# Performance work log

Measured on AMD Instinct MI355X. Metric: run time of the kernel, lower is better.

## Reference

```python
import jax, jax.numpy as jnp
import numpy as np

N_NODES = 100000
N_EDGES = 1600000
IN_C = 128
HID_C = 64
HEADS = 2
OUT_C = 40
NEG_SLOPE = 0.2  # PyG GATConv default


def setup_inputs() -> dict:
    key = jax.random.key(0)
    ks = jax.random.split(key, 10)
    x = jax.random.normal(ks[0], (N_NODES, IN_C), dtype=jnp.float32)
    edge_index = jax.random.randint(ks[1], (2, N_EDGES), 0, N_NODES, dtype=jnp.int32)
    # layer 1 params: Linear(in, heads*hid), att_src/att_dst [heads, hid], bias [heads*hid]
    s1 = 1.0 / np.sqrt(IN_C)
    W1 = jax.random.uniform(ks[2], (IN_C, HEADS * HID_C), minval=-s1, maxval=s1, dtype=jnp.float32)
    att_src1 = jax.random.normal(ks[3], (HEADS, HID_C), dtype=jnp.float32) * 0.1
    att_dst1 = jax.random.normal(ks[4], (HEADS, HID_C), dtype=jnp.float32) * 0.1
    b1 = jnp.zeros((HEADS * HID_C,), dtype=jnp.float32)
    # layer 2 params: Linear(heads*hid, out), heads=1, concat=False
    s2 = 1.0 / np.sqrt(HEADS * HID_C)
    W2 = jax.random.uniform(ks[5], (HEADS * HID_C, OUT_C), minval=-s2, maxval=s2, dtype=jnp.float32)
    att_src2 = jax.random.normal(ks[6], (1, OUT_C), dtype=jnp.float32) * 0.1
    att_dst2 = jax.random.normal(ks[7], (1, OUT_C), dtype=jnp.float32) * 0.1
    b2 = jnp.zeros((OUT_C,), dtype=jnp.float32)
    return {"x": x, "edge_index": edge_index, "W1": W1, "att_src1": att_src1,
            "att_dst1": att_dst1, "b1": b1, "W2": W2, "att_src2": att_src2,
            "att_dst2": att_dst2, "b2": b2}


def _gat_conv(x, src, dst, n, W, a_src, a_dst):
    # x: [N, F_in]; W: [F_in, H*C]; a_src/a_dst: [H, C]
    H, C = a_src.shape
    h = (x @ W).reshape(n, H, C)                       # [N, H, C]
    alpha_src = jnp.einsum('nhc,hc->nh', h, a_src)     # [N, H]
    alpha_dst = jnp.einsum('nhc,hc->nh', h, a_dst)
    e = alpha_src[src] + alpha_dst[dst]                # [E, H]
    e = jax.nn.leaky_relu(e, NEG_SLOPE)
    # numerically stable softmax over edges grouped by destination node
    m = jax.ops.segment_max(e, dst, num_segments=n)    # [N, H]
    ex = jnp.exp(e - m[dst])
    s = jax.ops.segment_sum(ex, dst, num_segments=n)
    coef = ex / (s[dst] + 1e-16)                       # [E, H]
    msg = h[src] * coef[:, :, None]                    # [E, H, C]
    return jax.ops.segment_sum(msg, dst, num_segments=n)  # [N, H, C]


def reference(x, edge_index, W1, att_src1, att_dst1, b1, W2, att_src2, att_dst2, b2):
    n = x.shape[0]
    # PyG GATConv adds self-loops by default
    loops = jnp.arange(n, dtype=edge_index.dtype)
    src = jnp.concatenate([edge_index[0], loops])
    dst = jnp.concatenate([edge_index[1], loops])
    # layer 1: heads=2, concat -> [N, H*C] + bias, then ELU
    h1 = _gat_conv(x, src, dst, n, W1, att_src1, att_dst1)
    h1 = h1.reshape(n, -1) + b1
    h1 = jax.nn.elu(h1)
    # layer 2: heads=1, concat=False -> mean over heads (=squeeze) + bias
    h2 = _gat_conv(h1, src, dst, n, W2, att_src2, att_dst2)
    h2 = h2.mean(axis=1) + b2
    return jax.nn.log_softmax(h2, axis=1)
```

## Files before the change

kernel.cpp:

```cpp
#include <hip/hip_runtime.h>
#include <hip/hip_fp16.h>
#include <math.h>

#define N_NODES 100000
#define N_EDGES 1600000
#define E_TOT   (N_EDGES + N_NODES)

#define NB     512
#define NPB    196
#define BCAP   4096
#define BIN_CH 4096
#define NBIN_WG ((E_TOT + BIN_CH - 1) / BIN_CH)

typedef __attribute__((ext_vector_type(8))) short short8v;
typedef __attribute__((ext_vector_type(4))) float float4v;

__device__ __forceinline__ float wexp(float v) {
    v = v > 0.f ? v : 0.2f * v;
    return __expf(v);
}

__device__ __forceinline__ unsigned short f2bf(float f) {
    unsigned u = __float_as_uint(f);
    return (unsigned short)((u + 0x7FFFu + ((u >> 16) & 1u)) >> 16);
}

__global__ __launch_bounds__(256) void xprep_k(
    const float* __restrict__ x, unsigned short* __restrict__ xb)
{
    int gid = blockIdx.x * 256 + threadIdx.x;
    float4 v = ((const float4*)x)[gid];
    ushort4 o;
    o.x = f2bf(v.x); o.y = f2bf(v.y); o.z = f2bf(v.z); o.w = f2bf(v.w);
    ((ushort4*)xb)[gid] = o;
}

__global__ __launch_bounds__(256) void w1prep_k(
    const float* __restrict__ W1, unsigned short* __restrict__ W1b)
{
    for (int idx = threadIdx.x; idx < 16384; idx += 256) {
        int i    = idx & 7;
        int lane = (idx >> 3) & 63;
        int f    = (idx >> 9) & 7;
        int ks   = idx >> 12;
        int k   = ks * 32 + (lane >> 4) * 8 + i;
        int col = f * 16 + (lane & 15);
        W1b[idx] = f2bf(W1[k * 128 + col]);
    }
}

__global__ __launch_bounds__(256) void gemm1_k(
    const unsigned short* __restrict__ xb, const unsigned short* __restrict__ W1b,
    const float* __restrict__ as1, const float* __restrict__ ad1,
    __half* __restrict__ h1h, float* __restrict__ asrc, float* __restrict__ adst)
{
    const int t = threadIdx.x;
    const int w = t >> 6, L = t & 63;
    const int lr = L & 15;
    const int lg = L >> 4;
    const int nbase = blockIdx.x * 64 + w * 16;

    float4v acc[8];
#pragma unroll
    for (int f = 0; f < 8; ++f) acc[f] = (float4v)0.f;

    int arow = nbase + lr; if (arow >= N_NODES) arow = N_NODES - 1;
    const unsigned short* xrow = xb + (size_t)arow * 128 + lg * 8;

#pragma unroll
    for (int ks = 0; ks < 4; ++ks) {
        short8v a = *(const short8v*)(xrow + ks * 32);
        const unsigned short* wb = W1b + ((size_t)ks * 8 * 64 + L) * 8;
#pragma unroll
        for (int f = 0; f < 8; ++f) {
            short8v b = *(const short8v*)(wb + (size_t)f * 512);
            acc[f] = __builtin_amdgcn_mfma_f32_16x16x32_bf16(a, b, acc[f], 0, 0, 0);
        }
    }

    float as_v[8], ad_v[8];
#pragma unroll
    for (int f = 0; f < 8; ++f) {
        as_v[f] = as1[f * 16 + lr];
        ad_v[f] = ad1[f * 16 + lr];
    }

#pragma unroll
    for (int r = 0; r < 4; ++r) {
        int node = nbase + lg * 4 + r;
        bool ok = node < N_NODES;
        if (ok) {
#pragma unroll
            for (int f = 0; f < 8; ++f)
                h1h[(size_t)node * 128 + f * 16 + lr] = __float2half_rn(acc[f][r]);
        }
        float ps0 = 0.f, pd0 = 0.f, ps1 = 0.f, pd1 = 0.f;
#pragma unroll
        for (int f = 0; f < 4; ++f) { ps0 += acc[f][r] * as_v[f]; pd0 += acc[f][r] * ad_v[f]; }
#pragma unroll
        for (int f = 4; f < 8; ++f) { ps1 += acc[f][r] * as_v[f]; pd1 += acc[f][r] * ad_v[f]; }
#pragma unroll
        for (int off = 1; off < 16; off <<= 1) {
            ps0 += __shfl_xor(ps0, off); pd0 += __shfl_xor(pd0, off);
            ps1 += __shfl_xor(ps1, off); pd1 += __shfl_xor(pd1, off);
        }
        if (lr == 0 && ok) {
            asrc[node * 2 + 0] = ps0; asrc[node * 2 + 1] = ps1;
            adst[node * 2 + 0] = pd0; adst[node * 2 + 1] = pd1;
        }
    }
}

__global__ __launch_bounds__(256) void bin_k(
    const int* __restrict__ ei, int* __restrict__ bcur, unsigned* __restrict__ bdata)
{
    __shared__ int hist[NB];
    __shared__ int base[NB];
    const int t = threadIdx.x;
    const int e0 = blockIdx.x * BIN_CH;

    int rs[16], rd[16];
#pragma unroll
    for (int p = 0; p < 16; ++p) {
        int e = e0 + p * 256 + t;
        if (e < E_TOT) {
            if (e < N_EDGES) { rs[p] = ei[e]; rd[p] = ei[N_EDGES + e]; }
            else             { rs[p] = rd[p] = e - N_EDGES; }
        } else rd[p] = -1;
    }

    for (int b = t; b < NB; b += 256) hist[b] = 0;
    __syncthreads();

#pragma unroll
    for (int p = 0; p < 16; ++p)
        if (rd[p] >= 0) atomicAdd(&hist[rd[p] / NPB], 1);
    __syncthreads();

    for (int b = t; b < NB; b += 256) {
        int c = hist[b];
        base[b] = c ? atomicAdd(&bcur[b], c) : 0;
        hist[b] = 0;
    }
    __syncthreads();

#pragma unroll
    for (int p = 0; p < 16; ++p) {
        if (rd[p] < 0) continue;
        int b  = rd[p] / NPB;
        int dl = rd[p] - b * NPB;
        int pos = base[b] + atomicAdd(&hist[b], 1);
        if (pos < BCAP)
            bdata[(size_t)b * BCAP + pos] = (unsigned)rs[p] | ((unsigned)dl << 17);
    }
}

__global__ __launch_bounds__(512) void scanb_k(
    const int* __restrict__ bcur, int* __restrict__ bbase)
{
    __shared__ int a[NB], b_[NB];
    int t = threadIdx.x;
    int v = bcur[t];
    a[t] = v;
    __syncthreads();
    int* src = a; int* dst = b_;
    for (int off = 1; off < NB; off <<= 1) {
        dst[t] = (t >= off) ? src[t - off] + src[t] : src[t];
        __syncthreads();
        int* tmp = src; src = dst; dst = tmp;
    }
    bbase[t] = src[t] - v;
}

__global__ __launch_bounds__(256) void build_k(
    const unsigned* __restrict__ bdata, const int* __restrict__ bcur,
    const int* __restrict__ bbase, int* __restrict__ row_start,
    int* __restrict__ csr_src)
{
    __shared__ unsigned rec[BCAP];
    __shared__ int hist[256];
    __shared__ int excl[NPB];
    __shared__ int lcur[NPB];
    const int t = threadIdx.x;
    const int b = blockIdx.x;
    const int cnt = min(bcur[b], BCAP);
    const int bb = bbase[b];

    hist[t] = 0;
    if (t < NPB) lcur[t] = 0;
    __syncthreads();

    for (int i = t; i < cnt; i += 256) {
        unsigned r = bdata[(size_t)b * BCAP + i];
        rec[i] = r;
        atomicAdd(&hist[r >> 17], 1);
    }
    __syncthreads();

    int v = hist[t];
    __syncthreads();
    for (int off = 1; off < 256; off <<= 1) {
        int y = (t >= off) ? hist[t - off] : 0;
        __syncthreads();
        hist[t] += y;
        __syncthreads();
    }
    if (t < NPB) excl[t] = hist[t] - v;
    __syncthreads();

    int node = b * NPB + t;
    if (t < NPB && node <= N_NODES) row_start[node] = bb + excl[t];

    for (int i = t; i < cnt; i += 256) {
        unsigned r = rec[i];
        int dl = r >> 17;
        int s  = r & 0x1FFFF;
        int slot = atomicAdd(&lcur[dl], 1);
        csr_src[bb + excl[dl] + slot] = s;
    }
}

__global__ __launch_bounds__(256) void fagg1_k(
    const int* __restrict__ csr_src, const int* __restrict__ row_start,
    const float* __restrict__ asrc, const float* __restrict__ adst,
    const __half* __restrict__ h1h, const float* __restrict__ b1,
    __half* __restrict__ out1h)
{
    int node = blockIdx.x * 4 + (threadIdx.x >> 6);
    int L = threadIdx.x & 63;
    int h = L >> 5;
    int b = row_start[node], e = row_start[node + 1];
    const float* as_h = asrc + h;
    float ad = adst[node * 2 + h];
    const __half2* H = (const __half2*)h1h;

    float2 a0 = make_float2(0.f, 0.f), a1 = a0, a2 = a0, a3 = a0;
    float d0 = 0.f, d1 = 0.f, d2 = 0.f, d3 = 0.f;

    int j = b;
    for (; j + 3 < e; j += 4) {
        int s0 = csr_src[j], s1 = csr_src[j + 1], s2 = csr_src[j + 2], s3 = csr_src[j + 3];
        float w0 = wexp(as_h[s0 * 2] + ad);
        float w1 = wexp(as_h[s1 * 2] + ad);
        float w2 = wexp(as_h[s2 * 2] + ad);
        float w3 = wexp(as_h[s3 * 2] + ad);
        float2 x0 = __half22float2(H[(size_t)s0 * 64 + L]);
        float2 x1 = __half22float2(H[(size_t)s1 * 64 + L]);
        float2 x2 = __half22float2(H[(size_t)s2 * 64 + L]);
        float2 x3 = __half22float2(H[(size_t)s3 * 64 + L]);
        a0.x += w0 * x0.x; a0.y += w0 * x0.y; d0 += w0;
        a1.x += w1 * x1.x; a1.y += w1 * x1.y; d1 += w1;
        a2.x += w2 * x2.x; a2.y += w2 * x2.y; d2 += w2;
        a3.x += w3 * x3.x; a3.y += w3 * x3.y; d3 += w3;
    }
    for (; j < e; ++j) {
        int s = csr_src[j];
        float w = wexp(as_h[s * 2] + ad);
        float2 xv = __half22float2(H[(size_t)s * 64 + L]);
        a0.x += w * xv.x; a0.y += w * xv.y; d0 += w;
    }

    float inv = 1.f / (((d0 + d1) + (d2 + d3)) + 1e-16f);
    float2 bb = ((const float2*)b1)[L];
    float vx = (a0.x + a1.x + a2.x + a3.x) * inv + bb.x;
    float vy = (a0.y + a1.y + a2.y + a3.y) * inv + bb.y;
    vx = vx > 0.f ? vx : expm1f(vx);
    vy = vy > 0.f ? vy : expm1f(vy);
    ((__half2*)(out1h + (size_t)node * 128))[L] = __floats2half2_rn(vx, vy);
}

__global__ __launch_bounds__(256) void gemm2_k(
    const __half* __restrict__ in1h, const float* __restrict__ W2,
    const float* __restrict__ as2, const float* __restrict__ ad2,
    __half* __restrict__ h2h, float* __restrict__ asrc, float* __restrict__ adst)
{
    __shared__ float xs[64][65];
    __shared__ float Wsh[64][64];
    __shared__ float as_s[64], ad_s[64];
    const int t = threadIdx.x;
    const int nbase = blockIdx.x * 64;
    const int c4 = t & 15;
    const int ng = t >> 4;

    if (t < 64) {
        as_s[t] = (t < 40) ? as2[t] : 0.f;
        ad_s[t] = (t < 40) ? ad2[t] : 0.f;
    }

    float acc[4][4];
#pragma unroll
    for (int i = 0; i < 4; ++i)
#pragma unroll
        for (int j = 0; j < 4; ++j) acc[i][j] = 0.f;

    for (int kt = 0; kt < 128; kt += 64) {
        __syncthreads();
        {
            int r = t >> 4;
            int c = (t & 15) * 4;
#pragma unroll
            for (int p = 0; p < 4; ++p) {
                int row = p * 16 + r;
                int gr = nbase + row; if (gr > N_NODES - 1) gr = N_NODES - 1;
                const __half2* src = (const __half2*)(in1h + (size_t)gr * 128 + kt + c);
                float2 f01 = __half22float2(src[0]);
                float2 f23 = __half22float2(src[1]);
                xs[row][c + 0] = f01.x; xs[row][c + 1] = f01.y;
                xs[row][c + 2] = f23.x; xs[row][c + 3] = f23.y;
            }
        }
        for (int i = t; i < 4096; i += 256) {
            int k = i >> 6, c = i & 63;
            Wsh[k][c] = (c < 40) ? W2[(size_t)(kt + k) * 40 + c] : 0.f;
        }
        __syncthreads();

#pragma unroll 4
        for (int k = 0; k < 64; ++k) {
            float4 w = *(const float4*)&Wsh[k][c4 * 4];
            float x0 = xs[ng * 4 + 0][k], x1 = xs[ng * 4 + 1][k];
            float x2 = xs[ng * 4 + 2][k], x3 = xs[ng * 4 + 3][k];
            acc[0][0] += x0 * w.x; acc[0][1] += x0 * w.y; acc[0][2] += x0 * w.z; acc[0][3] += x0 * w.w;
            acc[1][0] += x1 * w.x; acc[1][1] += x1 * w.y; acc[1][2] += x1 * w.z; acc[1][3] += x1 * w.w;
            acc[2][0] += x2 * w.x; acc[2][1] += x2 * w.y; acc[2][2] += x2 * w.z; acc[2][3] += x2 * w.w;
            acc[3][0] += x3 * w.x; acc[3][1] += x3 * w.y; acc[3][2] += x3 * w.z; acc[3][3] += x3 * w.w;
        }
    }

    float4 as4 = *(const float4*)&as_s[c4 * 4];
    float4 ad4 = *(const float4*)&ad_s[c4 * 4];
#pragma unroll
    for (int i = 0; i < 4; ++i) {
        int node = nbase + ng * 4 + i;
        float axx = acc[i][0], ayy = acc[i][1], azz = acc[i][2], aww = acc[i][3];
        if (node < N_NODES) {
            __half2* row = (__half2*)(h2h + (size_t)node * 64);
            row[2 * c4]     = __floats2half2_rn(axx, ayy);
            row[2 * c4 + 1] = __floats2half2_rn(azz, aww);
        }
        float ps = axx * as4.x + ayy * as4.y + azz * as4.z + aww * as4.w;
        float pd = axx * ad4.x + ayy * ad4.y + azz * ad4.z + aww * ad4.w;
#pragma unroll
        for (int off = 1; off < 16; off <<= 1) {
            ps += __shfl_xor(ps, off);
            pd += __shfl_xor(pd, off);
        }
        if ((t & 15) == 0 && node < N_NODES) {
            asrc[node] = ps;
            adst[node] = pd;
        }
    }
}

__global__ __launch_bounds__(256) void fagg2_k(
    const int* __restrict__ csr_src, const int* __restrict__ row_start,
    const float* __restrict__ asrc, const float* __restrict__ adst,
    const __half* __restrict__ h2h, const float* __restrict__ b2,
    float* __restrict__ out)
{
    int node = blockIdx.x * 4 + (threadIdx.x >> 6);
    int L = threadIdx.x & 63;
    bool act = L < 40;
    int col = act ? L : 0;
    int b = row_start[node], e = row_start[node + 1];
    float ad = adst[node];

    float a0 = 0.f, a1 = 0.f, a2 = 0.f, a3 = 0.f;
    float d0 = 0.f, d1 = 0.f, d2 = 0.f, d3 = 0.f;

    int j = b;
    for (; j + 3 < e; j += 4) {
        int s0 = csr_src[j], s1 = csr_src[j + 1], s2 = csr_src[j + 2], s3 = csr_src[j + 3];
        float w0 = wexp(asrc[s0] + ad);
        float w1 = wexp(asrc[s1] + ad);
        float w2 = wexp(asrc[s2] + ad);
        float w3 = wexp(asrc[s3] + ad);
        float x0 = __half2float(h2h[(size_t)s0 * 64 + col]);
        float x1 = __half2float(h2h[(size_t)s1 * 64 + col]);
        float x2 = __half2float(h2h[(size_t)s2 * 64 + col]);
        float x3 = __half2float(h2h[(size_t)s3 * 64 + col]);
        a0 += w0 * x0; d0 += w0;
        a1 += w1 * x1; d1 += w1;
        a2 += w2 * x2; d2 += w2;
        a3 += w3 * x3; d3 += w3;
    }
    for (; j < e; ++j) {
        int s = csr_src[j];
        float w = wexp(asrc[s] + ad);
        float xv = __half2float(h2h[(size_t)s * 64 + col]);
        a0 += w * xv; d0 += w;
    }

    float den = (d0 + d1) + (d2 + d3);
    float acc = (a0 + a1) + (a2 + a3);
    float v = act ? acc / (den + 1e-16f) + b2[L] : -1e30f;
    float mx = v;
#pragma unroll
    for (int off = 32; off; off >>= 1) mx = fmaxf(mx, __shfl_xor(mx, off));
    float ex = act ? __expf(v - mx) : 0.f;
#pragma unroll
    for (int off = 32; off; off >>= 1) ex += __shfl_xor(ex, off);
    if (act) out[(size_t)node * 40 + L] = v - mx - logf(ex);
}

extern "C" void kernel_launch(void* const* d_in, const int* in_sizes, int n_in,
                              void* d_out, int out_size, void* d_ws, size_t ws_size,
                              hipStream_t stream)
{
    const float* x   = (const float*)d_in[0];
    const int*   ei  = (const int*)d_in[1];
    const float* W1  = (const float*)d_in[2];
    const float* as1 = (const float*)d_in[3];
    const float* ad1 = (const float*)d_in[4];
    const float* b1  = (const float*)d_in[5];
    const float* W2  = (const float*)d_in[6];
    const float* as2 = (const float*)d_in[7];
    const float* ad2 = (const float*)d_in[8];
    const float* b2  = (const float*)d_in[9];
    float* out = (float*)d_out;

    float* ws = (float*)d_ws;
    __half* h1h   = (__half*)ws;
    __half* out1h = (__half*)(ws + 6400000);
    float* asrc1 = ws + 19200000;
    float* adst1 = ws + 19400000;
    float* asrc2 = ws + 19600000;
    float* adst2 = ws + 19700000;
    int* bcur      = (int*)(ws + 20110000);
    int* bbase     = (int*)(ws + 20111000);
    int* row_start = (int*)(ws + 20112000);
    int* csr_src   = (int*)(ws + 20220000);
    unsigned* bdata = (unsigned*)(ws + 22000000);
    unsigned short* xb  = (unsigned short*)(ws + 24100000);
    unsigned short* W1b = (unsigned short*)(ws + 27300000);

    hipMemsetAsync(bcur, 0, NB * sizeof(int), stream);

    xprep_k<<<12500, 256, 0, stream>>>(x, xb);
    w1prep_k<<<1, 256, 0, stream>>>(W1, W1b);

    bin_k<<<NBIN_WG, 256, 0, stream>>>(ei, bcur, bdata);
    scanb_k<<<1, 512, 0, stream>>>(bcur, bbase);
    build_k<<<NB, 256, 0, stream>>>(bdata, bcur, bbase, row_start, csr_src);

    gemm1_k<<<1563, 256, 0, stream>>>(xb, W1b, as1, ad1, h1h, asrc1, adst1);
    fagg1_k<<<25000, 256, 0, stream>>>(csr_src, row_start, asrc1, adst1, h1h, b1, out1h);

    __half* h2h = h1h;
    gemm2_k<<<1563, 256, 0, stream>>>(out1h, W2, as2, ad2, h2h, asrc2, adst2);
    fagg2_k<<<25000, 256, 0, stream>>>(csr_src, row_start, asrc2, adst2, h2h, b2, out);
}
```

Measured before the change: 286.1 us.

## Store node features in column panels and aggregate per panel for cache locality

The GEMM outputs are now written as column panels: 8 panels of 16 halves for layer 1 and 8 panels of 8 halves for layer 2. Each aggregation block processes only one panel, so the gathered working set per pass is small enough to stay in cache. Lanes also split edges across slots and finish with a shuffle reduction. The grid grows 8x, which recomputes edge weights and rereads the CSR arrays once per panel. Layer 2 adds a separate final kernel for bias and log-softmax, with an extra intermediate buffer round trip.

Result: slower. 856.4 us (+199.3%).

```diff
diff --git a/kernel.cpp b/kernel.cpp
--- a/kernel.cpp
+++ b/kernel.cpp
@@ -11,6 +11,9 @@
 #define BCAP   4096
 #define BIN_CH 4096
 #define NBIN_WG ((E_TOT + BIN_CH - 1) / BIN_CH)
+
+#define PAN1 (N_NODES * 16)
+#define PAN2 (N_NODES * 8)
 
 typedef __attribute__((ext_vector_type(8))) short short8v;
 typedef __attribute__((ext_vector_type(4))) float float4v;
@@ -52,7 +55,7 @@
 __global__ __launch_bounds__(256) void gemm1_k(
     const unsigned short* __restrict__ xb, const unsigned short* __restrict__ W1b,
     const float* __restrict__ as1, const float* __restrict__ ad1,
-    __half* __restrict__ h1h, float* __restrict__ asrc, float* __restrict__ adst)
+    __half* __restrict__ h1p, float* __restrict__ asrc, float* __restrict__ adst)
 {
     const int t = threadIdx.x;
     const int w = t >> 6, L = t & 63;
@@ -92,7 +95,7 @@
         if (ok) {
 #pragma unroll
             for (int f = 0; f < 8; ++f)
-                h1h[(size_t)node * 128 + f * 16 + lr] = __float2half_rn(acc[f][r]);
+                h1p[(size_t)f * PAN1 + (size_t)node * 16 + lr] = __float2half_rn(acc[f][r]);
         }
         float ps0 = 0.f, pd0 = 0.f, ps1 = 0.f, pd1 = 0.f;
 #pragma unroll
@@ -186,6 +189,8 @@
     const int cnt = min(bcur[b], BCAP);
     const int bb = bbase[b];
 
+    if (b == 0 && t < 16) csr_src[E_TOT + t] = 0;
+
     hist[t] = 0;
     if (t < NPB) lcur[t] = 0;
     __syncthreads();
@@ -223,56 +228,43 @@
 __global__ __launch_bounds__(256) void fagg1_k(
     const int* __restrict__ csr_src, const int* __restrict__ row_start,
     const float* __restrict__ asrc, const float* __restrict__ adst,
-    const __half* __restrict__ h1h, const float* __restrict__ b1,
+    const __half* __restrict__ h1p, const float* __restrict__ b1,
     __half* __restrict__ out1h)
 {
-    int node = blockIdx.x * 4 + (threadIdx.x >> 6);
-    int L = threadIdx.x & 63;
-    int h = L >> 5;
-    int b = row_start[node], e = row_start[node + 1];
+    const int slice = blockIdx.x & 7;
+    const int node = (blockIdx.x >> 3) * 4 + (threadIdx.x >> 6);
+    const int L = threadIdx.x & 63;
+    const int eslot = L >> 4, c16 = L & 15;
+    const int col = slice * 16 + c16;
+    const int h = col >> 6;
+    const int b = row_start[node], e = row_start[node + 1];
+    const float ad = adst[node * 2 + h];
     const float* as_h = asrc + h;
-    float ad = adst[node * 2 + h];
-    const __half2* H = (const __half2*)h1h;
-
-    float2 a0 = make_float2(0.f, 0.f), a1 = a0, a2 = a0, a3 = a0;
-    float d0 = 0.f, d1 = 0.f, d2 = 0.f, d3 = 0.f;
-
-    int j = b;
-    for (; j + 3 < e; j += 4) {
-        int s0 = csr_src[j], s1 = csr_src[j + 1], s2 = csr_src[j + 2], s3 = csr_src[j + 3];
-        float w0 = wexp(as_h[s0 * 2] + ad);
-        float w1 = wexp(as_h[s1 * 2] + ad);
-        float w2 = wexp(as_h[s2 * 2] + ad);
-        float w3 = wexp(as_h[s3 * 2] + ad);
-        float2 x0 = __half22float2(H[(size_t)s0 * 64 + L]);
-        float2 x1 = __half22float2(H[(size_t)s1 * 64 + L]);
-        float2 x2 = __half22float2(H[(size_t)s2 * 64 + L]);
-        float2 x3 = __half22float2(H[(size_t)s3 * 64 + L]);
-        a0.x += w0 * x0.x; a0.y += w0 * x0.y; d0 += w0;
-        a1.x += w1 * x1.x; a1.y += w1 * x1.y; d1 += w1;
-        a2.x += w2 * x2.x; a2.y += w2 * x2.y; d2 += w2;
-        a3.x += w3 * x3.x; a3.y += w3 * x3.y; d3 += w3;
-    }
-    for (; j < e; ++j) {
-        int s = csr_src[j];
-        float w = wexp(as_h[s * 2] + ad);
-        float2 xv = __half22float2(H[(size_t)s * 64 + L]);
-        a0.x += w * xv.x; a0.y += w * xv.y; d0 += w;
-    }
-
-    float inv = 1.f / (((d0 + d1) + (d2 + d3)) + 1e-16f);
-    float2 bb = ((const float2*)b1)[L];
-    float vx = (a0.x + a1.x + a2.x + a3.x) * inv + bb.x;
-    float vy = (a0.y + a1.y + a2.y + a3.y) * inv + bb.y;
-    vx = vx > 0.f ? vx : expm1f(vx);
-    vy = vy > 0.f ? vy : expm1f(vy);
-    ((__half2*)(out1h + (size_t)node * 128))[L] = __floats2half2_rn(vx, vy);
+    const __half* P = h1p + (size_t)slice * PAN1;
+
+    float acc = 0.f, den = 0.f;
+    for (int j = b; j < e; j += 4) {
+        int jj = j + eslot;
+        int s = csr_src[jj];
+        bool valid = jj < e;
+        float w = valid ? wexp(as_h[s * 2] + ad) : 0.f;
+        float x = __half2float(P[(size_t)s * 16 + c16]);
+        acc += w * x; den += w;
+    }
+
+    acc += __shfl_xor(acc, 16); acc += __shfl_xor(acc, 32);
+    den += __shfl_xor(den, 16); den += __shfl_xor(den, 32);
+
+    float v = acc / (den + 1e-16f) + b1[col];
+    v = v > 0.f ? v : expm1f(v);
+    if (eslot == 0)
+        out1h[(size_t)node * 128 + col] = __float2half_rn(v);
 }
 
 __global__ __launch_bounds__(256) void gemm2_k(
     const __half* __restrict__ in1h, const float* __restrict__ W2,
     const float* __restrict__ as2, const float* __restrict__ ad2,
-    __half* __restrict__ h2h, float* __restrict__ asrc, float* __restrict__ adst)
+    __half* __restrict__ h2p, float* __restrict__ asrc, float* __restrict__ adst)
 {
     __shared__ float xs[64][65];
     __shared__ float Wsh[64][64];
@@ -332,14 +324,17 @@
 #pragma unroll
     for (int i = 0; i < 4; ++i) {
         int node = nbase + ng * 4 + i;
-        float axx = acc[i][0], ayy = acc[i][1], azz = acc[i][2], aww = acc[i][3];
+        float av[4] = {acc[i][0], acc[i][1], acc[i][2], acc[i][3]};
         if (node < N_NODES) {
-            __half2* row = (__half2*)(h2h + (size_t)node * 64);
-            row[2 * c4]     = __floats2half2_rn(axx, ayy);
-            row[2 * c4 + 1] = __floats2half2_rn(azz, aww);
-        }
-        float ps = axx * as4.x + ayy * as4.y + azz * as4.z + aww * as4.w;
-        float pd = axx * ad4.x + ayy * ad4.y + azz * ad4.z + aww * ad4.w;
+#pragma unroll
+            for (int ii = 0; ii < 4; ++ii) {
+                int c = c4 * 4 + ii;
+                int p = c >> 3, off = c & 7;
+                h2p[(size_t)p * PAN2 + (size_t)node * 8 + off] = __float2half_rn(av[ii]);
+            }
+        }
+        float ps = av[0] * as4.x + av[1] * as4.y + av[2] * as4.z + av[3] * as4.w;
+        float pd = av[0] * ad4.x + av[1] * ad4.y + av[2] * ad4.z + av[3] * ad4.w;
 #pragma unroll
         for (int off = 1; off < 16; off <<= 1) {
             ps += __shfl_xor(ps, off);
@@ -355,45 +350,42 @@
 __global__ __launch_bounds__(256) void fagg2_k(
     const int* __restrict__ csr_src, const int* __restrict__ row_start,
     const float* __restrict__ asrc, const float* __restrict__ adst,
-    const __half* __restrict__ h2h, const float* __restrict__ b2,
+    const __half* __restrict__ h2p, float* __restrict__ h3)
+{
+    const int slice = blockIdx.x & 7;
+    const int node = (blockIdx.x >> 3) * 4 + (threadIdx.x >> 6);
+    const int L = threadIdx.x & 63;
+    const int eslot = L >> 3, c8 = L & 7;
+    const int col = slice * 8 + c8;
+    const int b = row_start[node], e = row_start[node + 1];
+    const float ad = adst[node];
+    const __half* P = h2p + (size_t)slice * PAN2;
+
+    float acc = 0.f, den = 0.f;
+    for (int j = b; j < e; j += 8) {
+        int jj = j + eslot;
+        int s = csr_src[jj];
+        bool valid = jj < e;
+        float w = valid ? wexp(asrc[s] + ad) : 0.f;
+        float x = __half2float(P[(size_t)s * 8 + c8]);
+        acc += w * x; den += w;
+    }
+
+    acc += __shfl_xor(acc, 8); acc += __shfl_xor(acc, 16); acc += __shfl_xor(acc, 32);
+    den += __shfl_xor(den, 8); den += __shfl_xor(den, 16); den += __shfl_xor(den, 32);
+
+    if (eslot == 0)
+        h3[(size_t)node * 64 + col] = acc / (den + 1e-16f);
+}
+
+__global__ __launch_bounds__(256) void final2_k(
+    const float* __restrict__ h3, const float* __restrict__ b2,
     float* __restrict__ out)
 {
     int node = blockIdx.x * 4 + (threadIdx.x >> 6);
     int L = threadIdx.x & 63;
     bool act = L < 40;
-    int col = act ? L : 0;
-    int b = row_start[node], e = row_start[node + 1];
-    float ad = adst[node];
-
-    float a0 = 0.f, a1 = 0.f, a2 = 0.f, a3 = 0.f;
-    float d0 = 0.f, d1 = 0.f, d2 = 0.f, d3 = 0.f;
-
-    int j = b;
-    for (; j + 3 < e; j += 4) {
-        int s0 = csr_src[j], s1 = csr_src[j + 1], s2 = csr_src[j + 2], s3 = csr_src[j + 3];
-        float w0 = wexp(asrc[s0] + ad);
-        float w1 = wexp(asrc[s1] + ad);
-        float w2 = wexp(asrc[s2] + ad);
-        float w3 = wexp(asrc[s3] + ad);
-        float x0 = __half2float(h2h[(size_t)s0 * 64 + col]);
-        float x1 = __half2float(h2h[(size_t)s1 * 64 + col]);
-        float x2 = __half2float(h2h[(size_t)s2 * 64 + col]);
-        float x3 = __half2float(h2h[(size_t)s3 * 64 + col]);
-        a0 += w0 * x0; d0 += w0;
-        a1 += w1 * x1; d1 += w1;
-        a2 += w2 * x2; d2 += w2;
-        a3 += w3 * x3; d3 += w3;
-    }
-    for (; j < e; ++j) {
-        int s = csr_src[j];
-        float w = wexp(asrc[s] + ad);
-        float xv = __half2float(h2h[(size_t)s * 64 + col]);
-        a0 += w * xv; d0 += w;
-    }
-
-    float den = (d0 + d1) + (d2 + d3);
-    float acc = (a0 + a1) + (a2 + a3);
-    float v = act ? acc / (den + 1e-16f) + b2[L] : -1e30f;
+    float v = act ? h3[(size_t)node * 64 + L] + b2[L] : -1e30f;
     float mx = v;
 #pragma unroll
     for (int off = 32; off; off >>= 1) mx = fmaxf(mx, __shfl_xor(mx, off));
@@ -420,19 +412,20 @@
     float* out = (float*)d_out;
 
     float* ws = (float*)d_ws;
-    __half* h1h   = (__half*)ws;
+    __half* h1p   = (__half*)ws;
     __half* out1h = (__half*)(ws + 6400000);
-    float* asrc1 = ws + 19200000;
-    float* adst1 = ws + 19400000;
-    float* asrc2 = ws + 19600000;
-    float* adst2 = ws + 19700000;
-    int* bcur      = (int*)(ws + 20110000);
-    int* bbase     = (int*)(ws + 20111000);
-    int* row_start = (int*)(ws + 20112000);
-    int* csr_src   = (int*)(ws + 20220000);
-    unsigned* bdata = (unsigned*)(ws + 22000000);
-    unsigned short* xb  = (unsigned short*)(ws + 24100000);
-    unsigned short* W1b = (unsigned short*)(ws + 27300000);
+    float* h3    = ws + 9600000;
+    float* asrc1 = ws + 16000000;
+    float* adst1 = ws + 16200000;
+    float* asrc2 = ws + 16400000;
+    float* adst2 = ws + 16500000;
+    int* bcur      = (int*)(ws + 16600000);
+    int* bbase     = (int*)(ws + 16601000);
+    int* row_start = (int*)(ws + 16602000);
+    int* csr_src   = (int*)(ws + 16710000);
+    unsigned* bdata = (unsigned*)(ws + 18500000);
+    unsigned short* xb  = (unsigned short*)(ws + 20600000);
+    unsigned short* W1b = (unsigned short*)(ws + 27000000);
 
     hipMemsetAsync(bcur, 0, NB * sizeof(int), stream);
 
@@ -443,10 +436,11 @@
     scanb_k<<<1, 512, 0, stream>>>(bcur, bbase);
     build_k<<<NB, 256, 0, stream>>>(bdata, bcur, bbase, row_start, csr_src);
 
-    gemm1_k<<<1563, 256, 0, stream>>>(xb, W1b, as1, ad1, h1h, asrc1, adst1);
-    fagg1_k<<<25000, 256, 0, stream>>>(csr_src, row_start, asrc1, adst1, h1h, b1, out1h);
-
-    __half* h2h = h1h;
-    gemm2_k<<<1563, 256, 0, stream>>>(out1h, W2, as2, ad2, h2h, asrc2, adst2);
-    fagg2_k<<<25000, 256, 0, stream>>>(csr_src, row_start, asrc2, adst2, h2h, b2, out);
-}
+    gemm1_k<<<1563, 256, 0, stream>>>(xb, W1b, as1, ad1, h1p, asrc1, adst1);
+    fagg1_k<<<200000, 256, 0, stream>>>(csr_src, row_start, asrc1, adst1, h1p, b1, out1h);
+
+    __half* h2p = h1p;
+    gemm2_k<<<1563, 256, 0, stream>>>(out1h, W2, as2, ad2, h2p, asrc2, adst2);
+    fagg2_k<<<200000, 256, 0, stream>>>(csr_src, row_start, asrc2, adst2, h2p, h3);
+    final2_k<<<25000, 256, 0, stream>>>(h3, b2, out);
+}
```

## Split layer-1 features into per-head panels and move layer-2 GEMM to MFMA

Applied to the files above, without the earlier changes.

Layer-1 features are stored as two per-head panels of 64 halves per node. The aggregation kernel now launches one block per head slice, with each half-wave taking alternate edges, and combines the two halves with a cross-lane shuffle. The aim is to shrink the working set each gather pass touches and give more edge-level parallelism. The layer-2 linear layer is rewritten from a scalar fp32 shared-memory GEMM to fp16 MFMA with a pre-swizzled weight buffer, padded from 40 to 48 columns. This trades an extra prep kernel, double the block count, and some half-precision rounding of weights for fewer FLOP cycles.

After: 345.6 us. 1.21x slower.

```diff
diff --git a/kernel.cpp b/kernel.cpp
--- a/kernel.cpp
+++ b/kernel.cpp
@@ -12,7 +12,10 @@
 #define BIN_CH 4096
 #define NBIN_WG ((E_TOT + BIN_CH - 1) / BIN_CH)
 
+#define PAN1H ((size_t)N_NODES * 64)
+
 typedef __attribute__((ext_vector_type(8))) short short8v;
+typedef __attribute__((ext_vector_type(8))) _Float16 half8v;
 typedef __attribute__((ext_vector_type(4))) float float4v;
 
 __device__ __forceinline__ float wexp(float v) {
@@ -49,10 +52,24 @@
     }
 }
 
+__global__ __launch_bounds__(256) void w2prep_k(
+    const float* __restrict__ W2, __half* __restrict__ W2h)
+{
+    for (int idx = threadIdx.x; idx < 6144; idx += 256) {
+        int i    = idx & 7;
+        int lane = (idx >> 3) & 63;
+        int rest = idx >> 9;
+        int f = rest % 3, ks = rest / 3;
+        int k   = ks * 32 + (lane >> 4) * 8 + i;
+        int col = f * 16 + (lane & 15);
+        W2h[idx] = __float2half_rn(col < 40 ? W2[k * 40 + col] : 0.f);
+    }
+}
+
 __global__ __launch_bounds__(256) void gemm1_k(
     const unsigned short* __restrict__ xb, const unsigned short* __restrict__ W1b,
     const float* __restrict__ as1, const float* __restrict__ ad1,
-    __half* __restrict__ h1h, float* __restrict__ asrc, float* __restrict__ adst)
+    __half* __restrict__ h1p, float* __restrict__ asrc, float* __restrict__ adst)
 {
     const int t = threadIdx.x;
     const int w = t >> 6, L = t & 63;
@@ -92,7 +109,8 @@
         if (ok) {
 #pragma unroll
             for (int f = 0; f < 8; ++f)
-                h1h[(size_t)node * 128 + f * 16 + lr] = __float2half_rn(acc[f][r]);
+                h1p[(size_t)(f >> 2) * PAN1H + (size_t)node * 64 + (f & 3) * 16 + lr]
+                    = __float2half_rn(acc[f][r]);
         }
         float ps0 = 0.f, pd0 = 0.f, ps1 = 0.f, pd1 = 0.f;
 #pragma unroll
@@ -223,31 +241,36 @@
 __global__ __launch_bounds__(256) void fagg1_k(
     const int* __restrict__ csr_src, const int* __restrict__ row_start,
     const float* __restrict__ asrc, const float* __restrict__ adst,
-    const __half* __restrict__ h1h, const float* __restrict__ b1,
+    const __half* __restrict__ h1p, const float* __restrict__ b1,
     __half* __restrict__ out1h)
 {
-    int node = blockIdx.x * 4 + (threadIdx.x >> 6);
-    int L = threadIdx.x & 63;
-    int h = L >> 5;
-    int b = row_start[node], e = row_start[node + 1];
-    const float* as_h = asrc + h;
-    float ad = adst[node * 2 + h];
-    const __half2* H = (const __half2*)h1h;
+    const int slice = blockIdx.x & 1;
+    const int node = (blockIdx.x >> 1) * 4 + (threadIdx.x >> 6);
+    const int L = threadIdx.x & 63;
+    const int eslot = L >> 5;
+    const int c32 = L & 31;
+    const int b = row_start[node], e = row_start[node + 1];
+    const float* as_h = asrc + slice;
+    const float ad = adst[node * 2 + slice];
+    const __half2* P = (const __half2*)(h1p + (size_t)slice * PAN1H);
 
     float2 a0 = make_float2(0.f, 0.f), a1 = a0, a2 = a0, a3 = a0;
     float d0 = 0.f, d1 = 0.f, d2 = 0.f, d3 = 0.f;
 
     int j = b;
-    for (; j + 3 < e; j += 4) {
-        int s0 = csr_src[j], s1 = csr_src[j + 1], s2 = csr_src[j + 2], s3 = csr_src[j + 3];
+    for (; j + 7 < e; j += 8) {
+        int s0 = csr_src[j + 0 + eslot];
+        int s1 = csr_src[j + 2 + eslot];
+        int s2 = csr_src[j + 4 + eslot];
+        int s3 = csr_src[j + 6 + eslot];
         float w0 = wexp(as_h[s0 * 2] + ad);
         float w1 = wexp(as_h[s1 * 2] + ad);
         float w2 = wexp(as_h[s2 * 2] + ad);
         float w3 = wexp(as_h[s3 * 2] + ad);
-        float2 x0 = __half22float2(H[(size_t)s0 * 64 + L]);
-        float2 x1 = __half22float2(H[(size_t)s1 * 64 + L]);
-        float2 x2 = __half22float2(H[(size_t)s2 * 64 + L]);
-        float2 x3 = __half22float2(H[(size_t)s3 * 64 + L]);
+        float2 x0 = __half22float2(P[(size_t)s0 * 32 + c32]);
+        float2 x1 = __half22float2(P[(size_t)s1 * 32 + c32]);
+        float2 x2 = __half22float2(P[(size_t)s2 * 32 + c32]);
+        float2 x3 = __half22float2(P[(size_t)s3 * 32 + c32]);
         a0.x += w0 * x0.x; a0.y += w0 * x0.y; d0 += w0;
         a1.x += w1 * x1.x; a1.y += w1 * x1.y; d1 += w1;
         a2.x += w2 * x2.x; a2.y += w2 * x2.y; d2 += w2;
@@ -255,97 +278,82 @@
     }
     for (; j < e; ++j) {
         int s = csr_src[j];
-        float w = wexp(as_h[s * 2] + ad);
-        float2 xv = __half22float2(H[(size_t)s * 64 + L]);
+        float w = (eslot == 0) ? wexp(as_h[s * 2] + ad) : 0.f;
+        float2 xv = __half22float2(P[(size_t)s * 32 + c32]);
         a0.x += w * xv.x; a0.y += w * xv.y; d0 += w;
     }
 
-    float inv = 1.f / (((d0 + d1) + (d2 + d3)) + 1e-16f);
-    float2 bb = ((const float2*)b1)[L];
-    float vx = (a0.x + a1.x + a2.x + a3.x) * inv + bb.x;
-    float vy = (a0.y + a1.y + a2.y + a3.y) * inv + bb.y;
+    float den = (d0 + d1) + (d2 + d3);
+    float sx  = (a0.x + a1.x) + (a2.x + a3.x);
+    float sy  = (a0.y + a1.y) + (a2.y + a3.y);
+    sx  += __shfl_xor(sx, 32);
+    sy  += __shfl_xor(sy, 32);
+    den += __shfl_xor(den, 32);
+
+    float inv = 1.f / (den + 1e-16f);
+    int col2 = slice * 32 + c32;
+    float2 bb = ((const float2*)b1)[col2];
+    float vx = sx * inv + bb.x;
+    float vy = sy * inv + bb.y;
     vx = vx > 0.f ? vx : expm1f(vx);
     vy = vy > 0.f ? vy : expm1f(vy);
-    ((__half2*)(out1h + (size_t)node * 128))[L] = __floats2half2_rn(vx, vy);
+    if (eslot == 0)
+        ((__half2*)(out1h + (size_t)node * 128))[col2] = __floats2half2_rn(vx, vy);
 }
 
 __global__ __launch_bounds__(256) void gemm2_k(
-    const __half* __restrict__ in1h, const float* __restrict__ W2,
+    const __half* __restrict__ out1h, const __half* __restrict__ W2h,
     const float* __restrict__ as2, const float* __restrict__ ad2,
     __half* __restrict__ h2h, float* __restrict__ asrc, float* __restrict__ adst)
 {
-    __shared__ float xs[64][65];
-    __shared__ float Wsh[64][64];
-    __shared__ float as_s[64], ad_s[64];
     const int t = threadIdx.x;
-    const int nbase = blockIdx.x * 64;
-    const int c4 = t & 15;
-    const int ng = t >> 4;
-
-    if (t < 64) {
-        as_s[t] = (t < 40) ? as2[t] : 0.f;
-        ad_s[t] = (t < 40) ? ad2[t] : 0.f;
-    }
-
-    float acc[4][4];
-#pragma unroll
-    for (int i = 0; i < 4; ++i)
-#pragma unroll
-        for (int j = 0; j < 4; ++j) acc[i][j] = 0.f;
-
-    for (int kt = 0; kt < 128; kt += 64) {
-        __syncthreads();
-        {
-            int r = t >> 4;
-            int c = (t & 15) * 4;
-#pragma unroll
-            for (int p = 0; p < 4; ++p) {
-                int row = p * 16 + r;
-                int gr = nbase + row; if (gr > N_NODES - 1) gr = N_NODES - 1;
-                const __half2* src = (const __half2*)(in1h + (size_t)gr * 128 + kt + c);
-                float2 f01 = __half22float2(src[0]);
-                float2 f23 = __half22float2(src[1]);
-                xs[row][c + 0] = f01.x; xs[row][c + 1] = f01.y;
-                xs[row][c + 2] = f23.x; xs[row][c + 3] = f23.y;
-            }
-        }
-        for (int i = t; i < 4096; i += 256) {
-            int k = i >> 6, c = i & 63;
-            Wsh[k][c] = (c < 40) ? W2[(size_t)(kt + k) * 40 + c] : 0.f;
-        }
-        __syncthreads();
-
-#pragma unroll 4
-        for (int k = 0; k < 64; ++k) {
-            float4 w = *(const float4*)&Wsh[k][c4 * 4];
-            float x0 = xs[ng * 4 + 0][k], x1 = xs[ng * 4 + 1][k];
-            float x2 = xs[ng * 4 + 2][k], x3 = xs[ng * 4 + 3][k];
-            acc[0][0] += x0 * w.x; acc[0][1] += x0 * w.y; acc[0][2] += x0 * w.z; acc[0][3] += x0 * w.w;
-            acc[1][0] += x1 * w.x; acc[1][1] += x1 * w.y; acc[1][2] += x1 * w.z; acc[1][3] += x1 * w.w;
-            acc[2][0] += x2 * w.x; acc[2][1] += x2 * w.y; acc[2][2] += x2 * w.z; acc[2][3] += x2 * w.w;
-            acc[3][0] += x3 * w.x; acc[3][1] += x3 * w.y; acc[3][2] += x3 * w.z; acc[3][3] += x3 * w.w;
-        }
-    }
-
-    float4 as4 = *(const float4*)&as_s[c4 * 4];
-    float4 ad4 = *(const float4*)&ad_s[c4 * 4];
-#pragma unroll
-    for (int i = 0; i < 4; ++i) {
-        int node = nbase + ng * 4 + i;
-        float axx = acc[i][0], ayy = acc[i][1], azz = acc[i][2], aww = acc[i][3];
-        if (node < N_NODES) {
-            __half2* row = (__half2*)(h2h + (size_t)node * 64);
-            row[2 * c4]     = __floats2half2_rn(axx, ayy);
-            row[2 * c4 + 1] = __floats2half2_rn(azz, aww);
-        }
-        float ps = axx * as4.x + ayy * as4.y + azz * as4.z + aww * as4.w;
-        float pd = axx * ad4.x + ayy * ad4.y + azz * ad4.z + aww * ad4.w;
+    const int w = t >> 6, L = t & 63;
+    const int lr = L & 15, lg = L >> 4;
+    const int nbase = blockIdx.x * 64 + w * 16;
+
+    float4v acc[3];
+#pragma unroll
+    for (int f = 0; f < 3; ++f) acc[f] = (float4v)0.f;
+
+    int arow = nbase + lr; if (arow >= N_NODES) arow = N_NODES - 1;
+    const __half* xrow = out1h + (size_t)arow * 128 + lg * 8;
+
+#pragma unroll
+    for (int ks = 0; ks < 4; ++ks) {
+        half8v a = *(const half8v*)(xrow + ks * 32);
+        const __half* wb = W2h + (size_t)ks * 1536 + (size_t)L * 8;
+#pragma unroll
+        for (int f = 0; f < 3; ++f) {
+            half8v bfr = *(const half8v*)(wb + (size_t)f * 512);
+            acc[f] = __builtin_amdgcn_mfma_f32_16x16x32_f16(a, bfr, acc[f], 0, 0, 0);
+        }
+    }
+
+    float as_v[3], ad_v[3];
+#pragma unroll
+    for (int f = 0; f < 3; ++f) {
+        int c = f * 16 + lr;
+        as_v[f] = (c < 40) ? as2[c] : 0.f;
+        ad_v[f] = (c < 40) ? ad2[c] : 0.f;
+    }
+
+#pragma unroll
+    for (int r = 0; r < 4; ++r) {
+        int node = nbase + lg * 4 + r;
+        bool ok = node < N_NODES;
+        if (ok) {
+#pragma unroll
+            for (int f = 0; f < 3; ++f)
+                h2h[(size_t)node * 64 + f * 16 + lr] = __float2half_rn(acc[f][r]);
+        }
+        float ps = acc[0][r] * as_v[0] + acc[1][r] * as_v[1] + acc[2][r] * as_v[2];
+        float pd = acc[0][r] * ad_v[0] + acc[1][r] * ad_v[1] + acc[2][r] * ad_v[2];
 #pragma unroll
         for (int off = 1; off < 16; off <<= 1) {
             ps += __shfl_xor(ps, off);
             pd += __shfl_xor(pd, off);
         }
-        if ((t & 15) == 0 && node < N_NODES) {
+        if (lr == 0 && ok) {
             asrc[node] = ps;
             adst[node] = pd;
         }
@@ -420,7 +428,7 @@
     float* out = (float*)d_out;
 
     float* ws = (float*)d_ws;
-    __half* h1h   = (__half*)ws;
+    __half* h1p   = (__half*)ws;
     __half* out1h = (__half*)(ws + 6400000);
     float* asrc1 = ws + 19200000;
     float* adst1 = ws + 19400000;
@@ -433,20 +441,22 @@
     unsigned* bdata = (unsigned*)(ws + 22000000);
     unsigned short* xb  = (unsigned short*)(ws + 24100000);
     unsigned short* W1b = (unsigned short*)(ws + 27300000);
+    __half* W2h = (__half*)(ws + 27310000);
 
     hipMemsetAsync(bcur, 0, NB * sizeof(int), stream);
 
     xprep_k<<<12500, 256, 0, stream>>>(x, xb);
     w1prep_k<<<1, 256, 0, stream>>>(W1, W1b);
+    w2prep_k<<<1, 256, 0, stream>>>(W2, W2h);
 
     bin_k<<<NBIN_WG, 256, 0, stream>>>(ei, bcur, bdata);
     scanb_k<<<1, 512, 0, stream>>>(bcur, bbase);
     build_k<<<NB, 256, 0, stream>>>(bdata, bcur, bbase, row_start, csr_src);
 
-    gemm1_k<<<1563, 256, 0, stream>>>(xb, W1b, as1, ad1, h1h, asrc1, adst1);
-    fagg1_k<<<25000, 256, 0, stream>>>(csr_src, row_start, asrc1, adst1, h1h, b1, out1h);
-
-    __half* h2h = h1h;
-    gemm2_k<<<1563, 256, 0, stream>>>(out1h, W2, as2, ad2, h2h, asrc2, adst2);
+    gemm1_k<<<1563, 256, 0, stream>>>(xb, W1b, as1, ad1, h1p, asrc1, adst1);
+    fagg1_k<<<50000, 256, 0, stream>>>(csr_src, row_start, asrc1, adst1, h1p, b1, out1h);
+
+    __half* h2h = (__half*)h1p;
+    gemm2_k<<<1563, 256, 0, stream>>>(out1h, W2h, as2, ad2, h2h, asrc2, adst2);
     fagg2_k<<<25000, 256, 0, stream>>>(csr_src, row_start, asrc2, adst2, h2h, b2, out);
 }
```
